# Optimization experiments

Hardware: AMD Instinct MI355X
Metric: run time of the kernel (lower is better)

## Reference

```python
import jax, jax.numpy as jnp
import numpy as np

LN_EPS = 1e-5

def _layernorm(x, g, b):
    mu = jnp.mean(x, axis=-1, keepdims=True)
    var = jnp.mean(jnp.square(x - mu), axis=-1, keepdims=True)
    return (x - mu) * jax.lax.rsqrt(var + LN_EPS) * g + b

def _mlp(x, W1, b1, W2, b2, W3, b3, g, b):
    # Linear+ReLU, Linear+ReLU, Linear, LayerNorm (n_hidden=2)
    x = jax.nn.relu(x @ W1 + b1)
    x = jax.nn.relu(x @ W2 + b2)
    x = x @ W3 + b3
    return _layernorm(x, g, b)

def setup_inputs() -> dict:
    key = jax.random.key(0)
    ks = jax.random.split(key, 20)
    N, E = 50000, 400000
    node_dim, edge_dim, hidden = 64, 32, 128
    msg_in = 2 * node_dim + edge_dim  # 160
    upd_in = 2 * node_dim             # 128

    def lin(k, din, dout):
        s = 1.0 / np.sqrt(din)
        return jax.random.uniform(k, (din, dout), jnp.float32, -s, s)

    inp = {
        "h": jax.random.normal(ks[0], (N, node_dim), jnp.float32),
        "edge_index": jax.random.randint(ks[1], (2, E), 0, N, jnp.int64 if jax.config.jax_enable_x64 else jnp.int32),
        "edge_attr": jax.random.normal(ks[2], (E, edge_dim), jnp.float32),
        # message MLP params
        "mW1": lin(ks[3], msg_in, hidden), "mb1": jnp.zeros((hidden,), jnp.float32),
        "mW2": lin(ks[4], hidden, hidden), "mb2": jnp.zeros((hidden,), jnp.float32),
        "mW3": lin(ks[5], hidden, node_dim), "mb3": jnp.zeros((node_dim,), jnp.float32),
        "mg": jnp.ones((node_dim,), jnp.float32), "mbeta": jnp.zeros((node_dim,), jnp.float32),
        # update MLP params
        "uW1": lin(ks[6], upd_in, hidden), "ub1": jnp.zeros((hidden,), jnp.float32),
        "uW2": lin(ks[7], hidden, hidden), "ub2": jnp.zeros((hidden,), jnp.float32),
        "uW3": lin(ks[8], hidden, node_dim), "ub3": jnp.zeros((node_dim,), jnp.float32),
        "ug": jnp.ones((node_dim,), jnp.float32), "ubeta": jnp.zeros((node_dim,), jnp.float32),
    }
    return inp

def reference(h, edge_index, edge_attr,
              mW1, mb1, mW2, mb2, mW3, mb3, mg, mbeta,
              uW1, ub1, uW2, ub2, uW3, ub3, ug, ubeta):
    N = h.shape[0]
    src, dst = edge_index[0], edge_index[1]
    # gather + concat: (E, 2*node_dim + edge_dim)
    msg_in = jnp.concatenate([h[src], h[dst], edge_attr], axis=-1)
    msg = _mlp(msg_in, mW1, mb1, mW2, mb2, mW3, mb3, mg, mbeta)  # (E, node_dim)
    agg = jax.ops.segment_sum(msg, dst, num_segments=N)          # (N, node_dim)
    h_new = _mlp(jnp.concatenate([h, agg], axis=-1),
                 uW1, ub1, uW2, ub2, uW3, ub3, ug, ubeta)
    h_new = h_new + h
    return (h_new, msg)
```

## Files before the change

kernel.cpp:

```cpp
#include <hip/hip_runtime.h>
#include <hip/hip_bf16.h>


typedef __attribute__((ext_vector_type(8))) short s16x8;
typedef __attribute__((ext_vector_type(4))) float f32x4;

__device__ __forceinline__ unsigned short f2bf(float x) {
  union { float f; unsigned u; } v; v.f = x;
  unsigned r = v.u + 0x7fffu + ((v.u >> 16) & 1u);
  return (unsigned short)(r >> 16);
}

__device__ __forceinline__ s16x8 ld_cvt8(const float* p) {
  float4 a = *(const float4*)p;
  float4 b = *(const float4*)(p + 4);
  union { s16x8 v; __hip_bfloat162 h2[4]; } u;
  float2 t;
  t.x = a.x; t.y = a.y; u.h2[0] = __float22bfloat162_rn(t);
  t.x = a.z; t.y = a.w; u.h2[1] = __float22bfloat162_rn(t);
  t.x = b.x; t.y = b.y; u.h2[2] = __float22bfloat162_rn(t);
  t.x = b.z; t.y = b.w; u.h2[3] = __float22bfloat162_rn(t);
  return u.v;
}

__global__ __launch_bounds__(256) void wconv(
    const float* __restrict__ mW1, const float* __restrict__ mW2, const float* __restrict__ mW3,
    const float* __restrict__ uW1, const float* __restrict__ uW2, const float* __restrict__ uW3,
    unsigned short* __restrict__ wts) {
  int t = blockIdx.x * 256 + threadIdx.x;
  const float* src; int K, N, off, base;
  if      (t < 20480) { src = mW1; K = 160; N = 128; off = 0;     base = 0;     }
  else if (t < 36864) { src = mW2; K = 128; N = 128; off = 20480; base = 21504; }
  else if (t < 45056) { src = mW3; K = 128; N = 64;  off = 36864; base = 37888; }
  else if (t < 61440) { src = uW1; K = 128; N = 128; off = 45056; base = 46080; }
  else if (t < 77824) { src = uW2; K = 128; N = 128; off = 61440; base = 62464; }
  else if (t < 86016) { src = uW3; K = 128; N = 64;  off = 77824; base = 78848; }
  else return;
  int local = t - off;
  int n = local / K, k = local - n * K;
  int idx;
  if (K == 160) idx = n * 168 + k;
  else          idx = base + n * 128 + ((((k >> 3) ^ (n & 7)) << 3) | (k & 7));
  wts[idx] = f2bf(src[k * N + n]);
}

__device__ __forceinline__ void stage_bias(float* bf, int tid, int nthr,
    const float* b1, const float* b2, const float* b3,
    const float* g, const float* bt) {
  for (int i = tid; i < 576; i += nthr) {
    float v = 0.f;
    if (i < 192)      { int c = i;       int l = c / 12, nt = c % 12; if (nt < 8) v = b1[nt * 16 + l]; }
    else if (i < 384) { int c = i - 192; int l = c / 12, nt = c % 12; if (nt < 8) v = b2[nt * 16 + l]; }
    else if (i < 448) { int c = i - 384; int l = c / 4,  nt = c % 4;  v = b3[nt * 16 + l]; }
    else if (i < 512) { int c = i - 448; int l = c / 4,  nt = c % 4;  v = g[nt * 16 + l]; }
    else              { int c = i - 512; int l = c / 4,  nt = c % 4;  v = bt[nt * 16 + l]; }
    bf[i] = v;
  }
}

__global__ __attribute__((amdgpu_flat_work_group_size(512, 512), amdgpu_waves_per_eu(4, 4)))
void msg_kernel(
    const float* __restrict__ h, const int* __restrict__ ei, const float* __restrict__ ea,
    const unsigned short* __restrict__ wts,
    const float* __restrict__ mb1, const float* __restrict__ mb2, const float* __restrict__ mb3,
    const float* __restrict__ mg, const float* __restrict__ mbt,
    float* __restrict__ msg_out, float* __restrict__ agg, int E) {
  __shared__ __align__(16) unsigned short lds[80000];
  const int tid = threadIdx.x;
  const int w = tid >> 6, lane = tid & 63, quad = lane >> 4, l15 = lane & 15;
  const int sw = l15 & 7;
  const int* srcI = ei;
  const int* dstI = ei + E;
  const int ntiles = (E + 31) >> 5;
  const int stride = gridDim.x * 8;
  int tile = blockIdx.x * 8 + w;

  for (int i = tid; i < 5760; i += 512)
    *(s16x8*)&lds[i * 8] = *(const s16x8*)&wts[i * 8];
  float* bf = (float*)&lds[78848];
  stage_bias(bf, tid, 512, mb1, mb2, mb3, mg, mbt);
  __syncthreads();

  unsigned short* act = &lds[46080 + w * 4096];
  const unsigned short* W1 = &lds[0];
  const unsigned short* W2 = &lds[21504];
  const unsigned short* W3 = &lds[37888];

  for (; tile < ntiles; tile += stride) {
    const int e0 = tile << 5;
    int ep1 = e0 + l15, ep2 = e0 + 16 + l15;
    int ec1 = ep1 < E ? ep1 : E - 1;
    int ec2 = ep2 < E ? ep2 : E - 1;
    int s1 = srcI[ec1], d1 = dstI[ec1];
    int s2 = srcI[ec2], d2 = dstI[ec2];
    const float* rs1 = h + (size_t)s1 * 64 + quad * 8;
    const float* rd1 = h + (size_t)d1 * 64 + quad * 8;
    const float* re1 = ea + (size_t)ec1 * 32 + quad * 8;
    const float* rs2 = h + (size_t)s2 * 64 + quad * 8;
    const float* rd2 = h + (size_t)d2 * 64 + quad * 8;
    const float* re2 = ea + (size_t)ec2 * 32 + quad * 8;
    s16x8 fa1[5], fa2[5];
    fa1[0] = ld_cvt8(rs1); fa1[1] = ld_cvt8(rs1 + 32);
    fa1[2] = ld_cvt8(rd1); fa1[3] = ld_cvt8(rd1 + 32);
    fa1[4] = ld_cvt8(re1);
    fa2[0] = ld_cvt8(rs2); fa2[1] = ld_cvt8(rs2 + 32);
    fa2[2] = ld_cvt8(rd2); fa2[3] = ld_cvt8(rd2 + 32);
    fa2[4] = ld_cvt8(re2);

    f32x4 aA[8], aB[8];
    #pragma unroll
    for (int nt = 0; nt < 8; nt++) { aA[nt] = (f32x4){0.f,0.f,0.f,0.f}; aB[nt] = (f32x4){0.f,0.f,0.f,0.f}; }
    #pragma unroll
    for (int kb = 0; kb < 5; kb++) {
      #pragma unroll
      for (int nt = 0; nt < 8; nt++) {
        s16x8 b = *(const s16x8*)&W1[(nt * 16 + l15) * 168 + kb * 32 + quad * 8];
        aA[nt] = __builtin_amdgcn_mfma_f32_16x16x32_bf16(fa1[kb], b, aA[nt], 0, 0, 0);
        aB[nt] = __builtin_amdgcn_mfma_f32_16x16x32_bf16(fa2[kb], b, aB[nt], 0, 0, 0);
      }
    }
    {
      union { float4 v[2]; float f[8]; } b1u;
      b1u.v[0] = *(const float4*)&bf[l15 * 12];
      b1u.v[1] = *(const float4*)&bf[l15 * 12 + 4];
      #pragma unroll
      for (int g = 0; g < 2; g++) {
        #pragma unroll
        for (int nt = 0; nt < 8; nt++) {
          int cb = 2 * nt + (l15 >> 3);
          #pragma unroll
          for (int r = 0; r < 4; r++) {
            int row = g * 16 + quad * 4 + r;
            int cbx = cb ^ (row & 7) ^ ((row >> 3) << 2);
            float v = (g ? aB[nt][r] : aA[nt][r]) + b1u.f[nt];
            v = v > 0.f ? v : 0.f;
            act[row * 128 + (cbx << 3) + sw] = f2bf(v);
          }
        }
      }
    }

    f32x4 cA[8], cB[8];
    #pragma unroll
    for (int nt = 0; nt < 8; nt++) { cA[nt] = (f32x4){0.f,0.f,0.f,0.f}; cB[nt] = (f32x4){0.f,0.f,0.f,0.f}; }
    const int hi1 = (l15 >> 3) << 2;
    const int hi2 = (2 + (l15 >> 3)) << 2;
    #pragma unroll
    for (int kb = 0; kb < 4; kb++) {
      int base = (kb << 2) + quad;
      s16x8 a1 = *(const s16x8*)&act[l15 * 128 + (((base ^ sw ^ hi1)) << 3)];
      s16x8 a2 = *(const s16x8*)&act[(16 + l15) * 128 + (((base ^ sw ^ hi2)) << 3)];
      int wblk = (base ^ sw) << 3;
      #pragma unroll
      for (int nt = 0; nt < 8; nt++) {
        s16x8 b = *(const s16x8*)&W2[(nt * 16 + l15) * 128 + wblk];
        cA[nt] = __builtin_amdgcn_mfma_f32_16x16x32_bf16(a1, b, cA[nt], 0, 0, 0);
        cB[nt] = __builtin_amdgcn_mfma_f32_16x16x32_bf16(a2, b, cB[nt], 0, 0, 0);
      }
    }
    {
      union { float4 v[2]; float f[8]; } b2u;
      b2u.v[0] = *(const float4*)&bf[192 + l15 * 12];
      b2u.v[1] = *(const float4*)&bf[192 + l15 * 12 + 4];
      #pragma unroll
      for (int g = 0; g < 2; g++) {
        #pragma unroll
        for (int nt = 0; nt < 8; nt++) {
          int cb = 2 * nt + (l15 >> 3);
          #pragma unroll
          for (int r = 0; r < 4; r++) {
            int row = g * 16 + quad * 4 + r;
            int cbx = cb ^ (row & 7) ^ ((row >> 3) << 2);
            float v = (g ? cB[nt][r] : cA[nt][r]) + b2u.f[nt];
            v = v > 0.f ? v : 0.f;
            act[row * 128 + (cbx << 3) + sw] = f2bf(v);
          }
        }
      }
    }

    f32x4 dA[4], dB[4];
    #pragma unroll
    for (int nt = 0; nt < 4; nt++) { dA[nt] = (f32x4){0.f,0.f,0.f,0.f}; dB[nt] = (f32x4){0.f,0.f,0.f,0.f}; }
    #pragma unroll
    for (int kb = 0; kb < 4; kb++) {
      int base = (kb << 2) + quad;
      s16x8 a1 = *(const s16x8*)&act[l15 * 128 + (((base ^ sw ^ hi1)) << 3)];
      s16x8 a2 = *(const s16x8*)&act[(16 + l15) * 128 + (((base ^ sw ^ hi2)) << 3)];
      int wblk = (base ^ sw) << 3;
      #pragma unroll
      for (int nt = 0; nt < 4; nt++) {
        s16x8 b = *(const s16x8*)&W3[(nt * 16 + l15) * 128 + wblk];
        dA[nt] = __builtin_amdgcn_mfma_f32_16x16x32_bf16(a1, b, dA[nt], 0, 0, 0);
        dB[nt] = __builtin_amdgcn_mfma_f32_16x16x32_bf16(a2, b, dB[nt], 0, 0, 0);
      }
    }

    {
      union { float4 v; float f[4]; } b3u, gu, btu;
      b3u.v = *(const float4*)&bf[384 + l15 * 4];
      gu.v  = *(const float4*)&bf[448 + l15 * 4];
      btu.v = *(const float4*)&bf[512 + l15 * 4];
      #pragma unroll
      for (int g = 0; g < 2; g++) {
        #pragma unroll
        for (int r = 0; r < 4; r++) {
          float v0 = (g ? dB[0][r] : dA[0][r]) + b3u.f[0];
          float v1 = (g ? dB[1][r] : dA[1][r]) + b3u.f[1];
          float v2 = (g ? dB[2][r] : dA[2][r]) + b3u.f[2];
          float v3 = (g ? dB[3][r] : dA[3][r]) + b3u.f[3];
          float p = v0 + v1 + v2 + v3;
          float q = v0 * v0 + v1 * v1 + v2 * v2 + v3 * v3;
          #pragma unroll
          for (int m = 1; m <= 8; m <<= 1) {
            p += __shfl_xor(p, m);
            q += __shfl_xor(q, m);
          }
          float mu = p * (1.f / 64.f);
          float var = q * (1.f / 64.f) - mu * mu;
          float rstd = rsqrtf(var + 1e-5f);
          int row = e0 + g * 16 + quad * 4 + r;
          if (row < E) {
            float o0 = (v0 - mu) * rstd * gu.f[0] + btu.f[0];
            float o1 = (v1 - mu) * rstd * gu.f[1] + btu.f[1];
            float o2 = (v2 - mu) * rstd * gu.f[2] + btu.f[2];
            float o3 = (v3 - mu) * rstd * gu.f[3] + btu.f[3];
            float* mp = msg_out + (size_t)row * 64 + l15;
            mp[0]  = o0;
            mp[16] = o1;
            mp[32] = o2;
            mp[48] = o3;
            int dd = __shfl(g ? d2 : d1, quad * 4 + r);
            float* ap = agg + (size_t)dd * 64 + l15;
            atomicAdd(ap,      o0);
            atomicAdd(ap + 16, o1);
            atomicAdd(ap + 32, o2);
            atomicAdd(ap + 48, o3);
          }
        }
      }
    }
  }
}

__global__ __attribute__((amdgpu_flat_work_group_size(1024, 1024), amdgpu_waves_per_eu(4, 4)))
void upd_kernel(
    const float* __restrict__ h, const float* __restrict__ agg,
    const unsigned short* __restrict__ wts,
    const float* __restrict__ ub1, const float* __restrict__ ub2, const float* __restrict__ ub3,
    const float* __restrict__ ug, const float* __restrict__ ubt,
    float* __restrict__ h_new, int Nn) {
  __shared__ __align__(16) unsigned short lds[74880];
  const int tid = threadIdx.x;
  const int w = tid >> 6, lane = tid & 63, quad = lane >> 4, l15 = lane & 15;
  const int sw = l15 & 7;
  const int ntiles = (Nn + 15) >> 4;
  const int stride = gridDim.x * 16;
  int tile = blockIdx.x * 16 + w;

  float4 P[8];
  if (tile < ntiles) {
    int n = (tile << 4) + l15; int nc = n < Nn ? n : 0;
    const float* rh = h + (size_t)nc * 64 + quad * 8;
    const float* rg = agg + (size_t)nc * 64 + quad * 8;
    P[0] = *(const float4*)rh;        P[1] = *(const float4*)(rh + 4);
    P[2] = *(const float4*)(rh + 32); P[3] = *(const float4*)(rh + 36);
    P[4] = *(const float4*)rg;        P[5] = *(const float4*)(rg + 4);
    P[6] = *(const float4*)(rg + 32); P[7] = *(const float4*)(rg + 36);
  }

  for (int i = tid; i < 5120; i += 1024)
    *(s16x8*)&lds[i * 8] = *(const s16x8*)&wts[46080 + i * 8];
  float* bf = (float*)&lds[73728];
  stage_bias(bf, tid, 1024, ub1, ub2, ub3, ug, ubt);
  __syncthreads();

  unsigned short* act = &lds[40960 + w * 2048];
  const unsigned short* W1 = &lds[0];
  const unsigned short* W2 = &lds[16384];
  const unsigned short* W3 = &lds[32768];

  for (; tile < ntiles; tile += stride) {
    const int n0 = tile << 4;
    s16x8 fa[4];
    {
      union { s16x8 v; __hip_bfloat162 h2[4]; } u0, u1, u2, u3;
      float2 t;
      t.x = P[0].x; t.y = P[0].y; u0.h2[0] = __float22bfloat162_rn(t);
      t.x = P[0].z; t.y = P[0].w; u0.h2[1] = __float22bfloat162_rn(t);
      t.x = P[1].x; t.y = P[1].y; u0.h2[2] = __float22bfloat162_rn(t);
      t.x = P[1].z; t.y = P[1].w; u0.h2[3] = __float22bfloat162_rn(t);
      t.x = P[2].x; t.y = P[2].y; u1.h2[0] = __float22bfloat162_rn(t);
      t.x = P[2].z; t.y = P[2].w; u1.h2[1] = __float22bfloat162_rn(t);
      t.x = P[3].x; t.y = P[3].y; u1.h2[2] = __float22bfloat162_rn(t);
      t.x = P[3].z; t.y = P[3].w; u1.h2[3] = __float22bfloat162_rn(t);
      t.x = P[4].x; t.y = P[4].y; u2.h2[0] = __float22bfloat162_rn(t);
      t.x = P[4].z; t.y = P[4].w; u2.h2[1] = __float22bfloat162_rn(t);
      t.x = P[5].x; t.y = P[5].y; u2.h2[2] = __float22bfloat162_rn(t);
      t.x = P[5].z; t.y = P[5].w; u2.h2[3] = __float22bfloat162_rn(t);
      t.x = P[6].x; t.y = P[6].y; u3.h2[0] = __float22bfloat162_rn(t);
      t.x = P[6].z; t.y = P[6].w; u3.h2[1] = __float22bfloat162_rn(t);
      t.x = P[7].x; t.y = P[7].y; u3.h2[2] = __float22bfloat162_rn(t);
      t.x = P[7].z; t.y = P[7].w; u3.h2[3] = __float22bfloat162_rn(t);
      fa[0] = u0.v; fa[1] = u1.v; fa[2] = u2.v; fa[3] = u3.v;
    }

    {
      int tn = tile + stride;
      if (tn < ntiles) {
        int n = (tn << 4) + l15; int nc = n < Nn ? n : 0;
        const float* rh = h + (size_t)nc * 64 + quad * 8;
        const float* rg = agg + (size_t)nc * 64 + quad * 8;
        P[0] = *(const float4*)rh;        P[1] = *(const float4*)(rh + 4);
        P[2] = *(const float4*)(rh + 32); P[3] = *(const float4*)(rh + 36);
        P[4] = *(const float4*)rg;        P[5] = *(const float4*)(rg + 4);
        P[6] = *(const float4*)(rg + 32); P[7] = *(const float4*)(rg + 36);
      }
    }

    f32x4 acc[8];
    #pragma unroll
    for (int nt = 0; nt < 8; nt++) acc[nt] = (f32x4){0.f, 0.f, 0.f, 0.f};
    #pragma unroll
    for (int kb = 0; kb < 4; kb++) {
      int blk8 = (((kb << 2) + quad) ^ sw) << 3;
      #pragma unroll
      for (int nt = 0; nt < 8; nt++) {
        s16x8 b = *(const s16x8*)&W1[(nt * 16 + l15) * 128 + blk8];
        acc[nt] = __builtin_amdgcn_mfma_f32_16x16x32_bf16(fa[kb], b, acc[nt], 0, 0, 0);
      }
    }
    {
      union { float4 v[2]; float f[8]; } b1u;
      b1u.v[0] = *(const float4*)&bf[l15 * 12];
      b1u.v[1] = *(const float4*)&bf[l15 * 12 + 4];
      #pragma unroll
      for (int nt = 0; nt < 8; nt++) {
        int cb = 2 * nt + (l15 >> 3);
        #pragma unroll
        for (int r = 0; r < 4; r++) {
          int row = quad * 4 + r;
          float v = acc[nt][r] + b1u.f[nt];
          v = v > 0.f ? v : 0.f;
          act[row * 128 + ((cb ^ (row & 7)) << 3) + sw] = f2bf(v);
        }
      }
    }

    f32x4 acc2[8];
    #pragma unroll
    for (int nt = 0; nt < 8; nt++) acc2[nt] = (f32x4){0.f, 0.f, 0.f, 0.f};
    #pragma unroll
    for (int kb = 0; kb < 4; kb++) {
      int blk8 = (((kb << 2) + quad) ^ sw) << 3;
      s16x8 a = *(const s16x8*)&act[l15 * 128 + blk8];
      #pragma unroll
      for (int nt = 0; nt < 8; nt++) {
        s16x8 b = *(const s16x8*)&W2[(nt * 16 + l15) * 128 + blk8];
        acc2[nt] = __builtin_amdgcn_mfma_f32_16x16x32_bf16(a, b, acc2[nt], 0, 0, 0);
      }
    }
    {
      union { float4 v[2]; float f[8]; } b2u;
      b2u.v[0] = *(const float4*)&bf[192 + l15 * 12];
      b2u.v[1] = *(const float4*)&bf[192 + l15 * 12 + 4];
      #pragma unroll
      for (int nt = 0; nt < 8; nt++) {
        int cb = 2 * nt + (l15 >> 3);
        #pragma unroll
        for (int r = 0; r < 4; r++) {
          int row = quad * 4 + r;
          float v = acc2[nt][r] + b2u.f[nt];
          v = v > 0.f ? v : 0.f;
          act[row * 128 + ((cb ^ (row & 7)) << 3) + sw] = f2bf(v);
        }
      }
    }

    f32x4 acc3[4];
    #pragma unroll
    for (int nt = 0; nt < 4; nt++) acc3[nt] = (f32x4){0.f, 0.f, 0.f, 0.f};
    #pragma unroll
    for (int kb = 0; kb < 4; kb++) {
      int blk8 = (((kb << 2) + quad) ^ sw) << 3;
      s16x8 a = *(const s16x8*)&act[l15 * 128 + blk8];
      #pragma unroll
      for (int nt = 0; nt < 4; nt++) {
        s16x8 b = *(const s16x8*)&W3[(nt * 16 + l15) * 128 + blk8];
        acc3[nt] = __builtin_amdgcn_mfma_f32_16x16x32_bf16(a, b, acc3[nt], 0, 0, 0);
      }
    }

    {
      union { float4 v; float f[4]; } b3u, gu, btu;
      b3u.v = *(const float4*)&bf[384 + l15 * 4];
      gu.v  = *(const float4*)&bf[448 + l15 * 4];
      btu.v = *(const float4*)&bf[512 + l15 * 4];
      #pragma unroll
      for (int r = 0; r < 4; r++) {
        float v0 = acc3[0][r] + b3u.f[0];
        float v1 = acc3[1][r] + b3u.f[1];
        float v2 = acc3[2][r] + b3u.f[2];
        float v3 = acc3[3][r] + b3u.f[3];
        float p = v0 + v1 + v2 + v3;
        float q = v0 * v0 + v1 * v1 + v2 * v2 + v3 * v3;
        #pragma unroll
        for (int m = 1; m <= 8; m <<= 1) {
          p += __shfl_xor(p, m);
          q += __shfl_xor(q, m);
        }
        float mu = p * (1.f / 64.f);
        float var = q * (1.f / 64.f) - mu * mu;
        float rstd = rsqrtf(var + 1e-5f);
        int row = n0 + quad * 4 + r;
        if (row < Nn) {
          const float* hp = h + (size_t)row * 64 + l15;
          float* op = h_new + (size_t)row * 64 + l15;
          op[0]  = (v0 - mu) * rstd * gu.f[0] + btu.f[0] + hp[0];
          op[16] = (v1 - mu) * rstd * gu.f[1] + btu.f[1] + hp[16];
          op[32] = (v2 - mu) * rstd * gu.f[2] + btu.f[2] + hp[32];
          op[48] = (v3 - mu) * rstd * gu.f[3] + btu.f[3] + hp[48];
        }
      }
    }
  }
}

extern "C" void kernel_launch(void* const* d_in, const int* in_sizes, int n_in,
                              void* d_out, int out_size, void* d_ws, size_t ws_size,
                              hipStream_t stream) {
  const float* h   = (const float*)d_in[0];
  const int*   ei  = (const int*)d_in[1];
  const float* ea  = (const float*)d_in[2];
  const float* mW1 = (const float*)d_in[3];
  const float* mb1 = (const float*)d_in[4];
  const float* mW2 = (const float*)d_in[5];
  const float* mb2 = (const float*)d_in[6];
  const float* mW3 = (const float*)d_in[7];
  const float* mb3 = (const float*)d_in[8];
  const float* mg  = (const float*)d_in[9];
  const float* mbt = (const float*)d_in[10];
  const float* uW1 = (const float*)d_in[11];
  const float* ub1 = (const float*)d_in[12];
  const float* uW2 = (const float*)d_in[13];
  const float* ub2 = (const float*)d_in[14];
  const float* uW3 = (const float*)d_in[15];
  const float* ub3 = (const float*)d_in[16];
  const float* ug  = (const float*)d_in[17];
  const float* ubt = (const float*)d_in[18];

  const int N = in_sizes[0] / 64;
  const int E = in_sizes[2] / 32;

  char* ws = (char*)d_ws;
  float* agg          = (float*)ws;              ws += (size_t)N * 64 * 4;
  unsigned short* wts = (unsigned short*)ws;     ws += 87040 * 2;

  float* h_new = (float*)d_out;
  float* msg   = (float*)d_out + (size_t)N * 64;

  hipMemsetAsync(agg, 0, (size_t)N * 64 * sizeof(float), stream);
  wconv<<<dim3((86016 + 255) / 256), dim3(256), 0, stream>>>(mW1, mW2, mW3, uW1, uW2, uW3, wts);
  msg_kernel<<<dim3(256), dim3(512), 0, stream>>>(
      h, ei, ea, wts, mb1, mb2, mb3, mg, mbt, msg, agg, E);
  upd_kernel<<<dim3(256), dim3(1024), 0, stream>>>(
      h, agg, wts, ub1, ub2, ub3, ug, ubt, h_new, N);
}
```

Before: 356.7 us.

## Prefetch next tile's edge indices and fold agg zeroing into weight conversion kernel

The message kernel now loads the src/dst indices for the next tile while the current tile is processed, and issues the first tile's index loads before the weight staging. This breaks the dependent index-then-gather load chain at the start of each iteration. Separately, the hipMemsetAsync of the aggregation buffer is removed, and the weight-conversion kernel now zeros it with extra threads, saving one launch. The trade-off is a few more live registers in the message kernel and a larger conversion grid.

```diff
diff --git a/kernel.cpp b/kernel.cpp
--- a/kernel.cpp
+++ b/kernel.cpp
@@ -26,16 +26,20 @@
 __global__ __launch_bounds__(256) void wconv(
     const float* __restrict__ mW1, const float* __restrict__ mW2, const float* __restrict__ mW3,
     const float* __restrict__ uW1, const float* __restrict__ uW2, const float* __restrict__ uW3,
-    unsigned short* __restrict__ wts) {
+    unsigned short* __restrict__ wts, float* __restrict__ agg, int aggv4) {
   int t = blockIdx.x * 256 + threadIdx.x;
+  if (t >= 86016) {
+    int i = t - 86016;
+    if (i < aggv4) ((float4*)agg)[i] = (float4){0.f, 0.f, 0.f, 0.f};
+    return;
+  }
   const float* src; int K, N, off, base;
   if      (t < 20480) { src = mW1; K = 160; N = 128; off = 0;     base = 0;     }
   else if (t < 36864) { src = mW2; K = 128; N = 128; off = 20480; base = 21504; }
   else if (t < 45056) { src = mW3; K = 128; N = 64;  off = 36864; base = 37888; }
   else if (t < 61440) { src = uW1; K = 128; N = 128; off = 45056; base = 46080; }
   else if (t < 77824) { src = uW2; K = 128; N = 128; off = 61440; base = 62464; }
-  else if (t < 86016) { src = uW3; K = 128; N = 64;  off = 77824; base = 78848; }
-  else return;
+  else                { src = uW3; K = 128; N = 64;  off = 77824; base = 78848; }
   int local = t - off;
   int n = local / K, k = local - n * K;
   int idx;
@@ -75,6 +79,15 @@
   const int stride = gridDim.x * 8;
   int tile = blockIdx.x * 8 + w;
 
+  int s1 = 0, d1 = 0, s2 = 0, d2 = 0;
+  if (tile < ntiles) {
+    int ep1 = (tile << 5) + l15, ep2 = (tile << 5) + 16 + l15;
+    int ec1 = ep1 < E ? ep1 : E - 1;
+    int ec2 = ep2 < E ? ep2 : E - 1;
+    s1 = srcI[ec1]; d1 = dstI[ec1];
+    s2 = srcI[ec2]; d2 = dstI[ec2];
+  }
+
   for (int i = tid; i < 5760; i += 512)
     *(s16x8*)&lds[i * 8] = *(const s16x8*)&wts[i * 8];
   float* bf = (float*)&lds[78848];
@@ -88,11 +101,8 @@
 
   for (; tile < ntiles; tile += stride) {
     const int e0 = tile << 5;
-    int ep1 = e0 + l15, ep2 = e0 + 16 + l15;
-    int ec1 = ep1 < E ? ep1 : E - 1;
-    int ec2 = ep2 < E ? ep2 : E - 1;
-    int s1 = srcI[ec1], d1 = dstI[ec1];
-    int s2 = srcI[ec2], d2 = dstI[ec2];
+    int ec1 = (e0 + l15) < E ? (e0 + l15) : E - 1;
+    int ec2 = (e0 + 16 + l15) < E ? (e0 + 16 + l15) : E - 1;
     const float* rs1 = h + (size_t)s1 * 64 + quad * 8;
     const float* rd1 = h + (size_t)d1 * 64 + quad * 8;
     const float* re1 = ea + (size_t)ec1 * 32 + quad * 8;
@@ -106,6 +116,18 @@
     fa2[0] = ld_cvt8(rs2); fa2[1] = ld_cvt8(rs2 + 32);
     fa2[2] = ld_cvt8(rd2); fa2[3] = ld_cvt8(rd2 + 32);
     fa2[4] = ld_cvt8(re2);
+
+    int s1n = 0, d1n = 0, s2n = 0, d2n = 0;
+    {
+      int tn = tile + stride;
+      if (tn < ntiles) {
+        int en1 = (tn << 5) + l15, en2 = (tn << 5) + 16 + l15;
+        int en1c = en1 < E ? en1 : E - 1;
+        int en2c = en2 < E ? en2 : E - 1;
+        s1n = srcI[en1c]; d1n = dstI[en1c];
+        s2n = srcI[en2c]; d2n = dstI[en2c];
+      }
+    }
 
     f32x4 aA[8], aB[8];
     #pragma unroll
@@ -240,6 +262,8 @@
         }
       }
     }
+
+    s1 = s1n; d1 = d1n; s2 = s2n; d2 = d2n;
   }
 }
 
@@ -459,8 +483,10 @@
   float* h_new = (float*)d_out;
   float* msg   = (float*)d_out + (size_t)N * 64;
 
-  hipMemsetAsync(agg, 0, (size_t)N * 64 * sizeof(float), stream);
-  wconv<<<dim3((86016 + 255) / 256), dim3(256), 0, stream>>>(mW1, mW2, mW3, uW1, uW2, uW3, wts);
+  const int aggv4 = N * 16;
+  const int wz_threads = 86016 + aggv4;
+  wconv<<<dim3((wz_threads + 255) / 256), dim3(256), 0, stream>>>(
+      mW1, mW2, mW3, uW1, uW2, uW3, wts, agg, aggv4);
   msg_kernel<<<dim3(256), dim3(512), 0, stream>>>(
       h, ei, ea, wts, mb1, mb2, mb3, mg, mbt, msg, agg, E);
   upd_kernel<<<dim3(256), dim3(1024), 0, stream>>>(
```

Result: faster. 321.9 us (-9.8%).
